# Kernel optimization log

Measured on AMD Instinct MI355X. Metric: run time of the kernel, lower is better.

Reference implementation:

```python
import jax, jax.numpy as jnp
import numpy as np

BN_EPS = 1e-5
TEMPERATURE = 256 ** 0.5  # sqrt(c2), since cv3 = ScaledDotProductAttention(c2)


def conv_bn_silu(x, w, gamma, beta, mean, var):
    # Conv2d(k=3, s=1, pad='same', bias=False) -> BatchNorm2d (running stats) -> SiLU
    y = jax.lax.conv_general_dilated(
        x, w, window_strides=(1, 1), padding='SAME',
        dimension_numbers=('NCHW', 'OIHW', 'NCHW'))
    scale = (gamma / jnp.sqrt(var + BN_EPS))[None, :, None, None]
    shift = (beta - mean * gamma / jnp.sqrt(var + BN_EPS))[None, :, None, None]
    y = y * scale + shift
    return y * jax.nn.sigmoid(y)  # SiLU


def setup_inputs() -> dict:
    key = jax.random.key(0)
    ks = jax.random.split(key, 8)
    B, C, H, W = 16, 256, 64, 64
    Ch = 128  # hidden channels c_ = int(c2 * e)
    x = jax.random.normal(ks[0], (B, C, H, W), dtype=jnp.float32)
    w1 = jax.random.normal(ks[1], (Ch, C, 3, 3), dtype=jnp.float32) * 0.05
    g1 = jnp.ones((Ch,), jnp.float32) + 0.1 * jax.random.normal(ks[2], (Ch,), dtype=jnp.float32)
    b1 = 0.1 * jax.random.normal(ks[3], (Ch,), dtype=jnp.float32)
    m1 = 0.1 * jax.random.normal(ks[4], (Ch,), dtype=jnp.float32)
    v1 = jnp.ones((Ch,), jnp.float32) + 0.5 * jax.random.uniform(ks[5], (Ch,), dtype=jnp.float32)
    w2 = jax.random.normal(ks[6], (C, Ch, 3, 3), dtype=jnp.float32) * 0.05
    g2 = jnp.ones((C,), jnp.float32)
    b2 = jnp.zeros((C,), jnp.float32)
    m2 = 0.1 * jax.random.normal(ks[7], (C,), dtype=jnp.float32)
    v2 = jnp.ones((C,), jnp.float32) + 0.5 * jax.random.uniform(jax.random.fold_in(key, 99), (C,), dtype=jnp.float32)
    return {"x": x, "w1": w1, "g1": g1, "b1": b1, "m1": m1, "v1": v1,
            "w2": w2, "g2": g2, "b2": b2, "m2": m2, "v2": v2}


def reference(x, w1, g1, b1, m1, v1, w2, g2, b2, m2, v2):
    y = conv_bn_silu(x, w1, g1, b1, m1, v1)       # [B, 128, H, W]
    y = conv_bn_silu(y, w2, g2, b2, m2, v2)       # [B, 256, H, W]
    B, C, H, W = y.shape
    q = y.reshape(B, C, H * W)                    # q = k^T = v, all views of y
    # channel-channel attention: scores [B, C, C]
    scores = jnp.einsum('bcn,bdn->bcd', q / TEMPERATURE, q)
    attn = jax.nn.softmax(scores, axis=-1)        # dropout is identity in eval
    out = jnp.einsum('bcd,bdn->bcn', attn, q).reshape(B, C, H, W)
    return x + out  # shortcut: c1 == c2
```

## Files before the change

### kernel.cpp

```cpp
#include <hip/hip_runtime.h>
#include <math.h>

#define BB 16
#define C1 256
#define CHD 128
#define NN 4096
#define INV_T (1.0f/16.0f)

typedef _Float16 half8 __attribute__((ext_vector_type(8)));
typedef __attribute__((ext_vector_type(4))) float f32x4;
typedef __attribute__((ext_vector_type(16))) float f32x16;

__device__ inline unsigned short f2h(float f) {
    _Float16 h = (_Float16)f;
    return __builtin_bit_cast(unsigned short, h);
}

#define GLDS(g, l) __builtin_amdgcn_global_load_lds(                              \
    (const __attribute__((address_space(1))) unsigned int*)(g),                   \
    (__attribute__((address_space(3))) unsigned int*)(l), 16, 0, 0)

__global__ __launch_bounds__(256) void nchw_to_nhwc_f16(
    const float* __restrict__ x, unsigned short* __restrict__ xh, int C)
{
    const int c0 = blockIdx.x * 64;
    const int hp = blockIdx.y;
    const int b  = blockIdx.z;
    const int nCk = C >> 4;

    if (hp == 0 || hp == 65) {
        for (int idx = threadIdx.x; idx < 1024; idx += 256) {
            int w = idx >> 4, cq = (idx & 15) * 4;
            ushort4 z; z.x = z.y = z.z = z.w = 0;
            *(ushort4*)&xh[((((size_t)b * nCk + (c0 >> 4) + (cq >> 4)) * 66 + hp) * 64 + w) * 16
                           + (cq & 15)] = z;
        }
        return;
    }
    const int h = hp - 1;
    __shared__ float ts[64][65];
    for (int idx = threadIdx.x; idx < 4096; idx += 256) {
        int cl = idx >> 6, w = idx & 63;
        ts[cl][w] = x[(((size_t)b * C + c0 + cl) * 64 + h) * 64 + w];
    }
    __syncthreads();
    for (int idx = threadIdx.x; idx < 1024; idx += 256) {
        int w = idx >> 4, cq = (idx & 15) * 4;
        ushort4 o;
        o.x = f2h(ts[cq + 0][w]); o.y = f2h(ts[cq + 1][w]);
        o.z = f2h(ts[cq + 2][w]); o.w = f2h(ts[cq + 3][w]);
        *(ushort4*)&xh[((((size_t)b * nCk + (c0 >> 4) + (cq >> 4)) * 66 + hp) * 64 + w) * 16
                       + (cq & 15)] = o;
    }
}

__global__ __launch_bounds__(256) void pack_w_kernel(
    const float* __restrict__ w, unsigned short* __restrict__ wT, int Cout, int Cin)
{
    int idx = blockIdx.x * 256 + threadIdx.x;
    int total = Cout * Cin * 9;
    if (idx >= total) return;
    int ci = idx % Cin; int t = idx / Cin; int co = t % Cout; int kk = t / Cout;
    wT[((((size_t)(ci >> 4)) * 9 + kk) * Cout + co) * 16 + (ci & 15)] =
        f2h(w[((size_t)co * Cin + ci) * 9 + kk]);
}

__global__ __launch_bounds__(256) void zero_y1h_pads(unsigned short* __restrict__ y1h)
{
    int idx = blockIdx.x * 256 + threadIdx.x;
    int b   = idx >> 12;
    int ck  = (idx >> 9) & 7;
    int row = ((idx >> 8) & 1) ? 65 : 0;
    int w   = (idx >> 2) & 63;
    int qtr = idx & 3;
    ushort4 z; z.x = z.y = z.z = z.w = 0;
    *(ushort4*)&y1h[((((size_t)b * 8 + ck) * 66 + row) * 64 + w) * 16 + qtr * 4] = z;
}

__global__ __launch_bounds__(512, 4) void conv_mfma_kernel(
    const unsigned short* __restrict__ xh, const unsigned short* __restrict__ wT,
    const float* __restrict__ gamma, const float* __restrict__ beta,
    const float* __restrict__ mean, const float* __restrict__ var,
    unsigned short* __restrict__ outNHWC,
    unsigned short* __restrict__ yhi, unsigned short* __restrict__ yhiT,
    int Cin, int Cout)
{
    const int tid  = threadIdx.x;
    const int wid  = tid >> 6;
    const int lane = tid & 63;
    const int l31  = lane & 31;
    const int hi   = lane >> 5;
    const int coBase = blockIdx.x * 64;
    const int h0     = blockIdx.y * 8;
    const int b      = blockIdx.z;
    const int nCk    = Cin >> 4;

    __shared__ __align__(16) unsigned short smem[39552];
    __shared__ float bnsc[64], bnsh[64];

    if (tid < 64) {
        int co = coBase + tid;
        float sc = gamma[co] * rsqrtf(var[co] + 1e-5f);
        bnsc[tid] = sc;
        bnsh[tid] = beta[co] - mean[co] * sc;
    }
    if (tid < 160) {
        int cell = tid >> 2;
        int part = tid & 3;
        int buf  = cell & 1;
        int col  = ((cell >> 1) & 1) ? 65 : 0;
        int r    = cell >> 2;
        ushort4 z; z.x = z.y = z.z = z.w = 0;
        *(ushort4*)&smem[buf * 10560 + (r * 66 + col) * 16 + part * 4] = z;
    }

    auto stage = [&](int sel, int ck) {
        unsigned short* wsd = smem + 21120 + sel * 9216;
        unsigned short* xsd = smem + sel * 10560;
        for (int it = wid; it < 38; it += 8) {
            if (it < 18) {
                int kk = it >> 1, h = it & 1;
                const unsigned short* g =
                    wT + (((size_t)ck * 9 + kk) * Cout + coBase + h * 32) * 16 + lane * 8;
                GLDS(g, wsd + (kk * 64 + h * 32) * 16);
            } else {
                int j = it - 18;
                int r = j >> 1, hf = j & 1;
                const unsigned short* g =
                    xh + ((((size_t)b * nCk + ck) * 66 + h0 + r) * 64 + hf * 32) * 16 + lane * 8;
                GLDS(g, xsd + (r * 66 + 1 + hf * 32) * 16);
            }
        }
    };

    stage(0, 0);
    __syncthreads();

    f32x16 acc[2][2] = {};

    int sel = 0;
    for (int ck = 0; ck < nCk; ck++) {
        if (ck + 1 < nCk) stage(sel ^ 1, ck + 1);

        const unsigned short* wsb = smem + 21120 + sel * 9216;
        const unsigned short* xsb = smem + sel * 10560;
#pragma unroll
        for (int kk = 0; kk < 9; kk++) {
            const int kh = kk / 3, kw = kk % 3;
            half8 a0 = *(const half8*)&wsb[(kk * 64 +      l31) * 16 + hi * 8];
            half8 a1 = *(const half8*)&wsb[(kk * 64 + 32 + l31) * 16 + hi * 8];
            const unsigned short* xr = &xsb[((wid + kh) * 66 + l31 + kw) * 16 + hi * 8];
            half8 b0 = *(const half8*)xr;
            half8 b1 = *(const half8*)&xr[32 * 16];
            acc[0][0] = __builtin_amdgcn_mfma_f32_32x32x16_f16(a0, b0, acc[0][0], 0, 0, 0);
            acc[0][1] = __builtin_amdgcn_mfma_f32_32x32x16_f16(a0, b1, acc[0][1], 0, 0, 0);
            acc[1][0] = __builtin_amdgcn_mfma_f32_32x32x16_f16(a1, b0, acc[1][0], 0, 0, 0);
            acc[1][1] = __builtin_amdgcn_mfma_f32_32x32x16_f16(a1, b1, acc[1][1], 0, 0, 0);
        }
        __syncthreads();
        sel ^= 1;
    }

    const int orow = h0 + wid;
    const bool isConv1 = (outNHWC != nullptr);

    __syncthreads();

#pragma unroll
    for (int mi = 0; mi < 2; mi++)
#pragma unroll
        for (int ni = 0; ni < 2; ni++) {
            f32x16 a = acc[mi][ni];
            int w = ni * 32 + l31;
            int swz = ((l31 + wid) & 7) << 3;
#pragma unroll
            for (int rq = 0; rq < 4; rq++) {
                int c0 = mi * 32 + rq * 8 + hi * 4;
                ushort4 o; unsigned short* op = (unsigned short*)&o;
#pragma unroll
                for (int r = 0; r < 4; r++) {
                    float t = a[rq * 4 + r] * bnsc[c0 + r] + bnsh[c0 + r];
                    float s = t / (1.f + __expf(-t));
                    op[r] = f2h(s);
                    if (!isConv1)
                        yhi[(((size_t)b * Cout + coBase + c0 + r) * 64 + orow) * 64 + w] = op[r];
                }
                *(ushort4*)&smem[wid * 4096 + w * 64 + (c0 ^ swz)] = o;
            }
        }
    __syncthreads();

    const int ckB = blockIdx.x * 4;
    const int nCkOut = Cout >> 4;
#pragma unroll
    for (int j = 0; j < 8; j++) {
        int g   = j * 512 + tid;
        int s   = g & 1;
        int w   = (g >> 1) & 63;
        int row = (g >> 7) & 7;
        int ck  = g >> 10;
        uint4 v = *(const uint4*)&smem[row * 4096 + w * 64 +
                     (((ck * 2 + s) * 8) ^ (((w + row) & 7) << 3))];
        if (isConv1) {
            *(uint4*)&outNHWC[((((size_t)b * nCkOut + ckB + ck) * 66 + h0 + row + 1) * 64 + w) * 16
                              + s * 8] = v;
        } else {
            *(uint4*)&yhiT[(((size_t)b * nCkOut + ckB + ck) * 4096 + (size_t)(h0 + row) * 64 + w) * 16
                           + s * 8] = v;
        }
    }
}

__global__ __launch_bounds__(256) void scores_mfma_kernel(
    const unsigned short* __restrict__ yhi, float* __restrict__ scores)
{
    static const int TI[10] = {0,0,0,0,1,1,1,2,2,3};
    static const int TJ[10] = {0,1,2,3,1,2,3,2,3,3};
    const int b  = blockIdx.z;
    const int ti = TI[blockIdx.x], tj = TJ[blockIdx.x];
    const int cB = ti * 64;
    const int dB = tj * 64;
    const int tid  = threadIdx.x;
    const int wid  = tid >> 6;
    const int lane = tid & 63;
    const int ln   = lane & 15;
    const int q    = lane >> 4;
    const int wm   = wid >> 1, wn = wid & 1;

    __shared__ unsigned short As[64 * 128];
    __shared__ unsigned short Bs[64 * 128];

    const int rl = lane >> 4;
    const int gl = lane & 15;

    f32x4 acc[2][2] = {};

    for (int ck = 0; ck < 32; ck++) {
        const int n0 = ck * 128;
        for (int it = wid; it < 32; it += 4) {
            const int tile = it >> 4;
            const int j = it & 15;
            const int r = j * 4 + rl;
            const int gq = gl ^ (r & 7);
            const int rowAbs = (tile ? dB : cB) + r;
            const unsigned short* g =
                yhi + ((size_t)b * 256 + rowAbs) * 4096 + n0 + gq * 8;
            GLDS(g, (tile ? Bs : As) + j * 512);
        }
        __syncthreads();

#pragma unroll
        for (int kwin = 0; kwin < 4; kwin++) {
            half8 ah[2], bh[2];
#pragma unroll
            for (int mi = 0; mi < 2; mi++) {
                int row = wm * 32 + mi * 16 + ln;
                ah[mi] = *(const half8*)&As[row * 128 + ((kwin * 4 + q) ^ (ln & 7)) * 8];
            }
#pragma unroll
            for (int ni = 0; ni < 2; ni++) {
                int row = wn * 32 + ni * 16 + ln;
                bh[ni] = *(const half8*)&Bs[row * 128 + ((kwin * 4 + q) ^ (ln & 7)) * 8];
            }
#pragma unroll
            for (int mi = 0; mi < 2; mi++)
#pragma unroll
                for (int ni = 0; ni < 2; ni++)
                    acc[mi][ni] = __builtin_amdgcn_mfma_f32_16x16x32_f16(
                        ah[mi], bh[ni], acc[mi][ni], 0, 0, 0);
        }
        __syncthreads();
    }

#pragma unroll
    for (int mi = 0; mi < 2; mi++)
#pragma unroll
        for (int ni = 0; ni < 2; ni++) {
            f32x4 a = acc[mi][ni];
            float vals[4];
            vals[0] = a.x * INV_T; vals[1] = a.y * INV_T;
            vals[2] = a.z * INV_T; vals[3] = a.w * INV_T;
            int c0 = cB + wm * 32 + mi * 16 + q * 4;
            int d  = dB + wn * 32 + ni * 16 + ln;
#pragma unroll
            for (int r = 0; r < 4; r++)
                scores[((size_t)b * C1 + c0 + r) * C1 + d] = vals[r];
            if (ti != tj) {
                float4 tv = {vals[0], vals[1], vals[2], vals[3]};
                *(float4*)&scores[((size_t)b * C1 + d) * C1 + c0] = tv;
            }
        }
}

__global__ __launch_bounds__(64) void softmax_kernel(
    const float* __restrict__ scores, unsigned short* __restrict__ attn16)
{
    const int row = blockIdx.x;
    const float* p = scores + (size_t)row * C1;
    const int lane = threadIdx.x;

    float4 v = ((const float4*)p)[lane];
    float m = fmaxf(fmaxf(v.x, v.y), fmaxf(v.z, v.w));
#pragma unroll
    for (int off = 32; off >= 1; off >>= 1)
        m = fmaxf(m, __shfl_xor(m, off, 64));

    float4 e;
    e.x = expf(v.x - m); e.y = expf(v.y - m);
    e.z = expf(v.z - m); e.w = expf(v.w - m);
    float s = e.x + e.y + e.z + e.w;
#pragma unroll
    for (int off = 32; off >= 1; off >>= 1)
        s += __shfl_xor(s, off, 64);
    float inv = 1.f / s;
    ushort4 o;
    o.x = f2h(e.x * inv); o.y = f2h(e.y * inv);
    o.z = f2h(e.z * inv); o.w = f2h(e.w * inv);
    *(ushort4*)&attn16[(size_t)row * C1 + lane * 4] = o;
}

__global__ __launch_bounds__(256) void out_mfma_kernel(
    const unsigned short* __restrict__ attn16, const unsigned short* __restrict__ yhiT,
    const float* __restrict__ x, float* __restrict__ out)
{
    const int b  = blockIdx.z;
    const int cB = blockIdx.y * 64;
    const int nB = blockIdx.x * 128;
    const int tid  = threadIdx.x;
    const int wid  = tid >> 6;
    const int lane = tid & 63;
    const int ln   = lane & 15;
    const int q    = lane >> 4;
    const int wm   = wid >> 1, wn = wid & 1;

    __shared__ unsigned short As[64 * 64];
    __shared__ unsigned short Bs[4 * 128 * 16];

    const int r8 = lane >> 3;
    const int gq = (lane & 7) ^ r8;

    f32x4 acc[2][4] = {};

    for (int ck = 0; ck < 4; ck++) {
        const int d0 = ck * 64;
        for (int it = wid; it < 24; it += 4) {
            if (it < 8) {
                const unsigned short* g =
                    attn16 + ((size_t)b * 256 + cB + it * 8 + r8) * 256 + d0 + gq * 8;
                GLDS(g, As + it * 512);
            } else {
                int j = it - 8;
                int u = j >> 2, part = j & 3;
                const unsigned short* g =
                    yhiT + (((size_t)b * 16 + ck * 4 + u) * 4096 + nB + part * 32) * 16 + lane * 8;
                GLDS(g, Bs + (u * 128 + part * 32) * 16);
            }
        }
        __syncthreads();

#pragma unroll
        for (int kwin = 0; kwin < 2; kwin++) {
            const int cc = (((kwin * 4 + q) ^ (ln & 7))) * 8;
            const int gK = kwin * 4 + q;
            half8 af[2], bfr[4];
#pragma unroll
            for (int mi = 0; mi < 2; mi++)
                af[mi] = *(const half8*)&As[(wm * 32 + mi * 16 + ln) * 64 + cc];
#pragma unroll
            for (int ni = 0; ni < 4; ni++) {
                int row = wn * 64 + ni * 16 + ln;
                bfr[ni] = *(const half8*)&Bs[(gK >> 1) * 2048 + row * 16 + (gK & 1) * 8];
            }
#pragma unroll
            for (int mi = 0; mi < 2; mi++)
#pragma unroll
                for (int ni = 0; ni < 4; ni++)
                    acc[mi][ni] = __builtin_amdgcn_mfma_f32_16x16x32_f16(
                        af[mi], bfr[ni], acc[mi][ni], 0, 0, 0);
        }
        __syncthreads();
    }

#pragma unroll
    for (int mi = 0; mi < 2; mi++)
#pragma unroll
        for (int ni = 0; ni < 4; ni++) {
            f32x4 a = acc[mi][ni];
            float vals[4] = {a.x, a.y, a.z, a.w};
#pragma unroll
            for (int r = 0; r < 4; r++) {
                int c = cB + wm * 32 + mi * 16 + q * 4 + r;
                int n = nB + wn * 64 + ni * 16 + ln;
                size_t o = ((size_t)b * C1 + c) * NN + n;
                out[o] = x[o] + vals[r];
            }
        }
}

extern "C" void kernel_launch(void* const* d_in, const int* in_sizes, int n_in,
                              void* d_out, int out_size, void* d_ws, size_t ws_size,
                              hipStream_t stream)
{
    const float* x  = (const float*)d_in[0];
    const float* w1 = (const float*)d_in[1];
    const float* g1 = (const float*)d_in[2];
    const float* b1 = (const float*)d_in[3];
    const float* m1 = (const float*)d_in[4];
    const float* v1 = (const float*)d_in[5];
    const float* w2 = (const float*)d_in[6];
    const float* g2 = (const float*)d_in[7];
    const float* b2 = (const float*)d_in[8];
    const float* m2 = (const float*)d_in[9];
    const float* v2 = (const float*)d_in[10];
    float* out = (float*)d_out;

    unsigned short* xh   = (unsigned short*)d_ws;
    unsigned short* y1h  = xh  + (size_t)17301504;
    unsigned short* wt1  = y1h + (size_t)8650752;
    unsigned short* wt2  = wt1 + (size_t)294912;
    unsigned short* yhiT = wt2 + (size_t)294912;
    unsigned short* yhi  = xh;
    float*          sc   = (float*)y1h;
    unsigned short* attn16 = (unsigned short*)(sc + 1048576);

    nchw_to_nhwc_f16<<<dim3(C1 / 64, 66, BB), 256, 0, stream>>>(x, xh, C1);
    pack_w_kernel<<<(9 * CHD * C1 + 255) / 256, 256, 0, stream>>>(w1, wt1, CHD, C1);
    pack_w_kernel<<<(9 * C1 * CHD + 255) / 256, 256, 0, stream>>>(w2, wt2, C1, CHD);
    zero_y1h_pads<<<256, 256, 0, stream>>>(y1h);

    conv_mfma_kernel<<<dim3(CHD / 64, 8, BB), 512, 0, stream>>>(
        xh, wt1, g1, b1, m1, v1, y1h, nullptr, nullptr, C1, CHD);
    conv_mfma_kernel<<<dim3(C1 / 64, 8, BB), 512, 0, stream>>>(
        y1h, wt2, g2, b2, m2, v2, nullptr, yhi, yhiT, CHD, C1);

    scores_mfma_kernel<<<dim3(10, 1, BB), 256, 0, stream>>>(yhi, sc);
    softmax_kernel<<<dim3(BB * C1), 64, 0, stream>>>(sc, attn16);
    out_mfma_kernel<<<dim3(NN / 128, 4, BB), 256, 0, stream>>>(attn16, yhiT, x, out);
}
```

Before: 326.1 us.

## Give each conv wave two output rows to reuse weight fragments across rows

The conv kernel now launches 256 threads (4 waves) instead of 512, with each wave computing two adjacent output rows. It loops over the four input rows, loading the B fragments once per input row and reusing each kernel-row's A fragments for both output rows, which cuts LDS reads per MFMA. The cost is double the accumulators (128 floats per lane), more register pressure, fewer waves per block to hide latency, and each wave issuing more global-to-LDS copies.

```diff
diff --git a/kernel.cpp b/kernel.cpp
--- a/kernel.cpp
+++ b/kernel.cpp
@@ -77,7 +77,7 @@
     *(ushort4*)&y1h[((((size_t)b * 8 + ck) * 66 + row) * 64 + w) * 16 + qtr * 4] = z;
 }
 
-__global__ __launch_bounds__(512, 4) void conv_mfma_kernel(
+__global__ __launch_bounds__(256, 2) void conv_mfma_kernel(
     const unsigned short* __restrict__ xh, const unsigned short* __restrict__ wT,
     const float* __restrict__ gamma, const float* __restrict__ beta,
     const float* __restrict__ mean, const float* __restrict__ var,
@@ -117,7 +117,7 @@
     auto stage = [&](int sel, int ck) {
         unsigned short* wsd = smem + 21120 + sel * 9216;
         unsigned short* xsd = smem + sel * 10560;
-        for (int it = wid; it < 38; it += 8) {
+        for (int it = wid; it < 38; it += 4) {
             if (it < 18) {
                 int kk = it >> 1, h = it & 1;
                 const unsigned short* g =
@@ -136,7 +136,8 @@
     stage(0, 0);
     __syncthreads();
 
-    f32x16 acc[2][2] = {};
+    f32x16 acc[2][2][2] = {};
+    const int lr = wid * 2;
 
     int sel = 0;
     for (int ck = 0; ck < nCk; ck++) {
@@ -144,57 +145,94 @@
 
         const unsigned short* wsb = smem + 21120 + sel * 9216;
         const unsigned short* xsb = smem + sel * 10560;
-#pragma unroll
-        for (int kk = 0; kk < 9; kk++) {
-            const int kh = kk / 3, kw = kk % 3;
-            half8 a0 = *(const half8*)&wsb[(kk * 64 +      l31) * 16 + hi * 8];
-            half8 a1 = *(const half8*)&wsb[(kk * 64 + 32 + l31) * 16 + hi * 8];
-            const unsigned short* xr = &xsb[((wid + kh) * 66 + l31 + kw) * 16 + hi * 8];
-            half8 b0 = *(const half8*)xr;
-            half8 b1 = *(const half8*)&xr[32 * 16];
-            acc[0][0] = __builtin_amdgcn_mfma_f32_32x32x16_f16(a0, b0, acc[0][0], 0, 0, 0);
-            acc[0][1] = __builtin_amdgcn_mfma_f32_32x32x16_f16(a0, b1, acc[0][1], 0, 0, 0);
-            acc[1][0] = __builtin_amdgcn_mfma_f32_32x32x16_f16(a1, b0, acc[1][0], 0, 0, 0);
-            acc[1][1] = __builtin_amdgcn_mfma_f32_32x32x16_f16(a1, b1, acc[1][1], 0, 0, 0);
+
+        half8 Aprev[2][3];
+#pragma unroll
+        for (int rr = 0; rr < 4; rr++) {
+            half8 bfr[2][3];
+#pragma unroll
+            for (int ni = 0; ni < 2; ni++)
+#pragma unroll
+                for (int kw = 0; kw < 3; kw++)
+                    bfr[ni][kw] = *(const half8*)
+                        &xsb[((lr + rr) * 66 + ni * 32 + l31 + kw) * 16 + hi * 8];
+
+            half8 Acur[2][3];
+            if (rr < 3) {
+#pragma unroll
+                for (int mi = 0; mi < 2; mi++)
+#pragma unroll
+                    for (int kw = 0; kw < 3; kw++)
+                        Acur[mi][kw] = *(const half8*)
+                            &wsb[((rr * 3 + kw) * 64 + mi * 32 + l31) * 16 + hi * 8];
+            }
+            if (rr < 3) {
+#pragma unroll
+                for (int kw = 0; kw < 3; kw++)
+#pragma unroll
+                    for (int mi = 0; mi < 2; mi++)
+#pragma unroll
+                        for (int ni = 0; ni < 2; ni++)
+                            acc[0][mi][ni] = __builtin_amdgcn_mfma_f32_32x32x16_f16(
+                                Acur[mi][kw], bfr[ni][kw], acc[0][mi][ni], 0, 0, 0);
+            }
+            if (rr >= 1) {
+#pragma unroll
+                for (int kw = 0; kw < 3; kw++)
+#pragma unroll
+                    for (int mi = 0; mi < 2; mi++)
+#pragma unroll
+                        for (int ni = 0; ni < 2; ni++)
+                            acc[1][mi][ni] = __builtin_amdgcn_mfma_f32_32x32x16_f16(
+                                Aprev[mi][kw], bfr[ni][kw], acc[1][mi][ni], 0, 0, 0);
+            }
+#pragma unroll
+            for (int mi = 0; mi < 2; mi++)
+#pragma unroll
+                for (int kw = 0; kw < 3; kw++)
+                    Aprev[mi][kw] = Acur[mi][kw];
         }
         __syncthreads();
         sel ^= 1;
     }
 
-    const int orow = h0 + wid;
     const bool isConv1 = (outNHWC != nullptr);
 
-    __syncthreads();
-
-#pragma unroll
-    for (int mi = 0; mi < 2; mi++)
-#pragma unroll
-        for (int ni = 0; ni < 2; ni++) {
-            f32x16 a = acc[mi][ni];
-            int w = ni * 32 + l31;
-            int swz = ((l31 + wid) & 7) << 3;
-#pragma unroll
-            for (int rq = 0; rq < 4; rq++) {
-                int c0 = mi * 32 + rq * 8 + hi * 4;
-                ushort4 o; unsigned short* op = (unsigned short*)&o;
-#pragma unroll
-                for (int r = 0; r < 4; r++) {
-                    float t = a[rq * 4 + r] * bnsc[c0 + r] + bnsh[c0 + r];
-                    float s = t / (1.f + __expf(-t));
-                    op[r] = f2h(s);
-                    if (!isConv1)
-                        yhi[(((size_t)b * Cout + coBase + c0 + r) * 64 + orow) * 64 + w] = op[r];
+#pragma unroll
+    for (int r2 = 0; r2 < 2; r2++) {
+        const int lrow = lr + r2;
+        const int orow = h0 + lrow;
+#pragma unroll
+        for (int mi = 0; mi < 2; mi++)
+#pragma unroll
+            for (int ni = 0; ni < 2; ni++) {
+                f32x16 a = acc[r2][mi][ni];
+                int w = ni * 32 + l31;
+                int swz = ((l31 + lrow) & 7) << 3;
+#pragma unroll
+                for (int rq = 0; rq < 4; rq++) {
+                    int c0 = mi * 32 + rq * 8 + hi * 4;
+                    ushort4 o; unsigned short* op = (unsigned short*)&o;
+#pragma unroll
+                    for (int r = 0; r < 4; r++) {
+                        float t = a[rq * 4 + r] * bnsc[c0 + r] + bnsh[c0 + r];
+                        float s = t / (1.f + __expf(-t));
+                        op[r] = f2h(s);
+                        if (!isConv1)
+                            yhi[(((size_t)b * Cout + coBase + c0 + r) * 64 + orow) * 64 + w]
+                                = op[r];
+                    }
+                    *(ushort4*)&smem[lrow * 4096 + w * 64 + (c0 ^ swz)] = o;
                 }
-                *(ushort4*)&smem[wid * 4096 + w * 64 + (c0 ^ swz)] = o;
-            }
-        }
+            }
+    }
     __syncthreads();
 
     const int ckB = blockIdx.x * 4;
     const int nCkOut = Cout >> 4;
 #pragma unroll
-    for (int j = 0; j < 8; j++) {
-        int g   = j * 512 + tid;
+    for (int j = 0; j < 16; j++) {
+        int g   = j * 256 + tid;
         int s   = g & 1;
         int w   = (g >> 1) & 63;
         int row = (g >> 7) & 7;
@@ -428,9 +466,9 @@
     pack_w_kernel<<<(9 * C1 * CHD + 255) / 256, 256, 0, stream>>>(w2, wt2, C1, CHD);
     zero_y1h_pads<<<256, 256, 0, stream>>>(y1h);
 
-    conv_mfma_kernel<<<dim3(CHD / 64, 8, BB), 512, 0, stream>>>(
+    conv_mfma_kernel<<<dim3(CHD / 64, 8, BB), 256, 0, stream>>>(
         xh, wt1, g1, b1, m1, v1, y1h, nullptr, nullptr, C1, CHD);
-    conv_mfma_kernel<<<dim3(C1 / 64, 8, BB), 512, 0, stream>>>(
+    conv_mfma_kernel<<<dim3(C1 / 64, 8, BB), 256, 0, stream>>>(
         y1h, wt2, g2, b2, m2, v2, nullptr, yhi, yhiT, CHD, C1);
 
     scores_mfma_kernel<<<dim3(10, 1, BB), 256, 0, stream>>>(yhi, sc);
```

Result: slower. 333.2 us (+2.2%).
